# Kernel tuning notes

Measured on AMD Instinct MI355X. Metric: run time of the kernel, lower is better.

## Reference

```python
import jax, jax.numpy as jnp
import numpy as np

N_NODES = 10000
N_EDGES = 160000
N_GRAPHS = 20
IN_F, HID, OUT_F, HEADS = 50, 256, 121, 4
NEG_SLOPE = 0.2
GN_EPS = 1e-5
SM_EPS = 1e-16


def _with_self_loops(edge_index, n):
    loop = jnp.arange(n, dtype=edge_index.dtype)
    src = jnp.concatenate([edge_index[0], loop])
    dst = jnp.concatenate([edge_index[1], loop])
    return src, dst


def gat_conv(x, W, att_src, att_dst, bias, src, dst, heads, out_c):
    # PyG GATConv: linear -> per-node attention halves -> edge leaky_relu
    # -> softmax over incoming edges of each dst -> weighted scatter-sum.
    n = x.shape[0]
    h = (x @ W).reshape(n, heads, out_c)                # [N,H,C]
    a_s = (h * att_src).sum(-1)                          # [N,H]
    a_d = (h * att_dst).sum(-1)                          # [N,H]
    e = a_s[src] + a_d[dst]                              # [E,H]
    e = jnp.where(e > 0, e, NEG_SLOPE * e)
    e_max = jax.ops.segment_max(e, dst, num_segments=n)  # self-loops cover all dst
    ex = jnp.exp(e - e_max[dst])
    den = jax.ops.segment_sum(ex, dst, num_segments=n)
    alpha = ex / (den[dst] + SM_EPS)                     # [E,H]
    out = jax.ops.segment_sum(h[src] * alpha[..., None], dst, num_segments=n)
    return out.reshape(n, heads * out_c) + bias


def graph_norm(x, batch, weight, bias, mean_scale, n_graphs):
    cnt = jax.ops.segment_sum(jnp.ones((x.shape[0],), x.dtype), batch,
                              num_segments=n_graphs)[:, None]    # [G,1]
    mean = jax.ops.segment_sum(x, batch, num_segments=n_graphs) / cnt
    ctr = x - mean[batch] * mean_scale
    var = jax.ops.segment_sum(ctr * ctr, batch, num_segments=n_graphs) / cnt
    inv = jax.lax.rsqrt(var + GN_EPS)
    return weight * ctr * inv[batch] + bias


def setup_inputs() -> dict:
    key = jax.random.key(0)
    ks = jax.random.split(key, 24)
    d = {}
    d['x'] = jax.random.normal(ks[0], (N_NODES, IN_F), jnp.float32)
    d['edge_index'] = jax.random.randint(ks[1], (2, N_EDGES), 0, N_NODES, jnp.int64 if jax.config.jax_enable_x64 else jnp.int32)
    d['batch'] = jnp.sort(jax.random.randint(ks[2], (N_NODES,), 0, N_GRAPHS))
    def glorot(k, shape):
        fan = shape[0] + shape[-1]
        return jax.random.normal(k, shape, jnp.float32) * np.sqrt(2.0 / fan)
    dims = [(IN_F, HEADS, HID), (HEADS * HID, HEADS, HID), (HEADS * HID, HEADS, HID), (HEADS * HID, 1, OUT_F)]
    i = 3
    for li, (fin, h, c) in enumerate(dims, 1):
        d[f'W{li}'] = glorot(ks[i], (fin, h * c)); i += 1
        d[f'as{li}'] = glorot(ks[i], (h, c)); i += 1
        d[f'ad{li}'] = glorot(ks[i], (h, c)); i += 1
        d[f'b{li}'] = jnp.zeros((h * c,), jnp.float32)
    for li in (1, 2, 3):
        w = HEADS * HID
        d[f'gw{li}'] = jnp.ones((w,), jnp.float32)
        d[f'gb{li}'] = jnp.zeros((w,), jnp.float32)
        d[f'ga{li}'] = jnp.ones((w,), jnp.float32)
    return d


def reference(x, edge_index, batch,
              W1, as1, ad1, b1, W2, as2, ad2, b2, W3, as3, ad3, b3, W4, as4, ad4, b4,
              gw1, gb1, ga1, gw2, gb2, ga2, gw3, gb3, ga3):
    src, dst = _with_self_loops(edge_index, N_NODES)
    h = gat_conv(x, W1, as1, ad1, b1, src, dst, HEADS, HID)
    h = jax.nn.elu(graph_norm(h, batch, gw1, gb1, ga1, N_GRAPHS))
    h = gat_conv(h, W2, as2, ad2, b2, src, dst, HEADS, HID)
    h = jax.nn.elu(graph_norm(h, batch, gw2, gb2, ga2, N_GRAPHS))
    h = gat_conv(h, W3, as3, ad3, b3, src, dst, HEADS, HID)
    h = jax.nn.elu(graph_norm(h, batch, gw3, gb3, ga3, N_GRAPHS))
    return gat_conv(h, W4, as4, ad4, b4, src, dst, 1, OUT_F)
```

## Files before the change

### kernel.cpp

```cpp
#include <hip/hip_runtime.h>
#include <math.h>

#define NN 10000
#define NE 160000
#define E2 (NE + NN)
#define NG 20
#define MPAD 10240
#define NSPLIT 8

typedef __attribute__((ext_vector_type(8))) short short8;
typedef __attribute__((ext_vector_type(4))) float f32x4;
typedef __attribute__((ext_vector_type(4))) unsigned short us4;

__device__ inline unsigned short f2bf(float f){
  unsigned u = __float_as_uint(f);
  unsigned r = u + 0x7FFFu + ((u >> 16) & 1u);
  return (unsigned short)(r >> 16);
}
__device__ inline float bf2f(unsigned short h){ return __uint_as_float(((unsigned)h) << 16); }

__device__ inline void gload_lds16(const void* g, void* l){
  __builtin_amdgcn_global_load_lds((const __attribute__((address_space(1))) void*)g,
                                   (__attribute__((address_space(3))) void*)l, 16, 0, 0);
}

__global__ void k_gptr(const int* __restrict__ batch, int* __restrict__ gptr){
  int g = threadIdx.x;
  if (g > NG) return;
  int lo = 0, hi = NN;
  while (lo < hi){ int mid = (lo+hi)>>1; if (batch[mid] < g) lo = mid+1; else hi = mid; }
  gptr[g] = lo;
}

__global__ void k_count(const int* __restrict__ ei, int* __restrict__ cnt){
  int e = blockIdx.x*256 + threadIdx.x;
  if (e >= E2) return;
  int d = (e < NE) ? ei[NE + e] : (e - NE);
  atomicAdd(&cnt[d], 1);
}

__global__ void k_scan(const int* __restrict__ cnt, int* __restrict__ ptr){
  __shared__ int tpre[256];
  __shared__ int tsum[256];
  int tid = threadIdx.x;
  const int per = (NN + 255)/256;
  int base = tid*per;
  int s = 0;
  for (int i=0;i<per;i++){ int idx=base+i; if (idx<NN) s += cnt[idx]; }
  tsum[tid] = s;
  __syncthreads();
  if (tid == 0){
    int run = 0;
    for (int i=0;i<256;i++){ tpre[i]=run; run += tsum[i]; }
    ptr[NN] = run;
  }
  __syncthreads();
  int run = tpre[tid];
  for (int i=0;i<per;i++){ int idx=base+i; if (idx<NN){ ptr[idx]=run; run += cnt[idx]; } }
}

__global__ void k_copy(const int* __restrict__ src, int* __restrict__ dst){
  int i = blockIdx.x*256 + threadIdx.x;
  if (i < NN) dst[i] = src[i];
}

__global__ void k_scatter(const int* __restrict__ ei, int* __restrict__ fill, int* __restrict__ csrc){
  int e = blockIdx.x*256 + threadIdx.x;
  if (e >= E2) return;
  int s, d;
  if (e < NE){ s = ei[e]; d = ei[NE + e]; } else { s = d = e - NE; }
  int pos = atomicAdd(&fill[d], 1);
  csrc[pos] = s;
}

__global__ void k_xconv(const float* __restrict__ x, unsigned short* __restrict__ xbf){
  int i = blockIdx.x*256 + threadIdx.x;
  if (i >= MPAD*64) return;
  int r = i >> 6, c = i & 63;
  float v = (r < NN && c < 50) ? x[r*50 + c] : 0.f;
  xbf[i] = f2bf(v);
}

#define WT0 0
#define WT1 65536
#define WT2 1114112
#define WT3 2162688
#define WTT 2293760
__global__ void k_wconvall(const float* __restrict__ W0, const float* __restrict__ W1,
                           const float* __restrict__ W2, const float* __restrict__ W3,
                           unsigned short* __restrict__ wt){
  int i = blockIdx.x*256 + threadIdx.x;
  if (i >= WTT) return;
  const float* W; int K, N, Kpad, off;
  if (i < WT1){ W=W0; K=50; N=1024; Kpad=64; off=WT0; }
  else if (i < WT2){ W=W1; K=1024; N=1024; Kpad=1024; off=WT1; }
  else if (i < WT3){ W=W2; K=1024; N=1024; Kpad=1024; off=WT2; }
  else { W=W3; K=1024; N=121; Kpad=1024; off=WT3; }
  int j = i - off;
  int nn = j / Kpad, kk = j - nn*Kpad;
  float v = (nn < N && kk < K) ? W[(size_t)kk*N + nn] : 0.f;
  wt[i] = f2bf(v);
}

__global__ void k_attpad4(const float* __restrict__ AS3, const float* __restrict__ AD3,
                          float* __restrict__ asp4, float* __restrict__ adp4){
  int i = threadIdx.x;
  asp4[i] = (i < 121) ? AS3[i] : 0.f;
  adp4[i] = (i < 121) ? AD3[i] : 0.f;
}

template<int TBN>
__global__ __launch_bounds__(512, 2) void k_gemm256(
    const unsigned short* __restrict__ A,
    const unsigned short* __restrict__ Bt,
    unsigned short* __restrict__ Cbf,
    const float* __restrict__ asp, const float* __restrict__ adp,
    float* __restrict__ a_s, float* __restrict__ a_d,
    int M, int K, int FS, int ncb, int H)
{
  constexpr int MFR = 8;
  constexpr int NFR = TBN/64;
  constexpr int ABYTES = 256*64;
  constexpr int BBYTES = TBN*64;
  constexpr int AINST = 2;
  constexpr int BINST = TBN/128;
  constexpr int LPS = AINST + BINST;
  __shared__ unsigned short sA[3*256*32];
  __shared__ unsigned short sB[3*TBN*32];
  const int tid = threadIdx.x;
  const int wave = tid >> 6;
  const int lane = tid & 63;
  const int nwg = gridDim.x;
  const int q = nwg >> 3, rmod = nwg & 7;
  const int xcd = blockIdx.x & 7, idx = blockIdx.x >> 3;
  const int wg = (xcd < rmod) ? (xcd*(q+1) + idx) : (rmod*(q+1) + (xcd - rmod)*q + idx);
  const int rowt = wg / ncb;
  const int colt = wg - rowt*ncb;
  const int row0 = rowt * 256;
  const int col0 = colt * TBN;
  const int wr = (wave >> 2) * 128;
  const int wc = (wave & 3) * (TBN/4);
  f32x4 acc[MFR][NFR];
  #pragma unroll
  for (int i=0;i<MFR;i++)
    #pragma unroll
    for (int j=0;j<NFR;j++){ acc[i][j][0]=0.f; acc[i][j][1]=0.f; acc[i][j][2]=0.f; acc[i][j][3]=0.f; }

  const unsigned short* aP[AINST];
  int aL[AINST];
  #pragma unroll
  for (int i=0;i<AINST;i++){
    int s = (wave*AINST + i)*64 + lane;
    int row = s >> 2, chn = (s & 3) ^ ((row >> 1) & 3);
    aP[i] = A + (size_t)(row0 + row)*K + chn*8;
    aL[i] = (wave*AINST + i)*1024;
  }
  const unsigned short* bP[BINST];
  int bL[BINST];
  #pragma unroll
  for (int i=0;i<BINST;i++){
    int s = (wave*BINST + i)*64 + lane;
    int row = s >> 2, chn = (s & 3) ^ ((row >> 1) & 3);
    bP[i] = Bt + (size_t)(col0 + row)*K + chn*8;
    bL[i] = (wave*BINST + i)*1024;
  }
  char* ldsA = (char*)sA;
  char* ldsB = (char*)sB;

  auto STAGE = [&](int k0, int buf){
    #pragma unroll
    for (int i=0;i<AINST;i++) gload_lds16(aP[i] + k0, ldsA + buf*ABYTES + aL[i]);
    #pragma unroll
    for (int i=0;i<BINST;i++) gload_lds16(bP[i] + k0, ldsB + buf*BBYTES + bL[i]);
  };

  const int NT = K >> 5;
  const int kch = lane >> 4;
  const int rlo = lane & 15;

  STAGE(0, 0);
  STAGE(32, 1);

  int cur = 0;
  for (int t = 0; t < NT; ++t){
    asm volatile("s_waitcnt lgkmcnt(0)" ::: "memory");
    if (t+1 < NT){
      if constexpr (LPS==4) asm volatile("s_waitcnt vmcnt(4)" ::: "memory");
      else                  asm volatile("s_waitcnt vmcnt(3)" ::: "memory");
    } else {
      asm volatile("s_waitcnt vmcnt(0)" ::: "memory");
    }
    __builtin_amdgcn_sched_barrier(0);
    __builtin_amdgcn_s_barrier();
    __builtin_amdgcn_sched_barrier(0);
    const unsigned short* bA = sA + cur*(256*32);
    const unsigned short* bB = sB + cur*(TBN*32);
    short8 af[MFR], bfr[NFR];
    #pragma unroll
    for (int m=0;m<MFR;m++){
      int r = wr + m*16 + rlo;
      af[m] = *(const short8*)(bA + r*32 + ((kch ^ ((r>>1)&3))<<3));
    }
    #pragma unroll
    for (int n=0;n<NFR;n++){
      int r = wc + n*16 + rlo;
      bfr[n] = *(const short8*)(bB + r*32 + ((kch ^ ((r>>1)&3))<<3));
    }
    if (t+2 < NT){
      int nb = cur + 2; if (nb >= 3) nb -= 3;
      STAGE((t+2) << 5, nb);
    }
    __builtin_amdgcn_s_setprio(1);
    #pragma unroll
    for (int m=0;m<MFR;m++)
      #pragma unroll
      for (int n=0;n<NFR;n++)
        acc[m][n] = __builtin_amdgcn_mfma_f32_16x16x32_bf16(af[m], bfr[n], acc[m][n], 0, 0, 0);
    __builtin_amdgcn_s_setprio(0);
    cur += 1; if (cur == 3) cur = 0;
  }
  const int cr = (lane >> 4) * 4;
  const int cc = lane & 15;
  #pragma unroll
  for (int m=0;m<MFR;m++){
    #pragma unroll
    for (int n=0;n<NFR;n++){
      int col = col0 + wc + n*16 + cc;
      #pragma unroll
      for (int r=0;r<4;r++){
        int row = row0 + wr + m*16 + cr + r;
        if (row < M) Cbf[(size_t)row*FS + col] = f2bf(acc[m][n][r]);
      }
    }
  }
  float asv[NFR], adv[NFR];
  #pragma unroll
  for (int n=0;n<NFR;n++){
    int col = col0 + wc + n*16 + cc;
    asv[n] = asp[col]; adv[n] = adp[col];
  }
  __syncthreads();
  float* part = (float*)sA;
  #pragma unroll
  for (int m=0;m<MFR;m++){
    #pragma unroll
    for (int r=0;r<4;r++){
      float ss = 0.f, sd = 0.f;
      #pragma unroll
      for (int n=0;n<NFR;n++){ float v = acc[m][n][r]; ss += v*asv[n]; sd += v*adv[n]; }
      #pragma unroll
      for (int o=8;o;o>>=1){ ss += __shfl_xor(ss,o); sd += __shfl_xor(sd,o); }
      if (cc == 0){
        int rowLocal = m*16 + cr + r;
        int pidx = ((wave>>2)*128 + rowLocal)*8 + (wave&3)*2;
        part[pidx] = ss; part[pidx+1] = sd;
      }
    }
  }
  __syncthreads();
  {
    int row = tid >> 1, v = tid & 1;
    int base = row*8 + v;
    float s = part[base] + part[base+2] + part[base+4] + part[base+6];
    int grow = row0 + row;
    const int head = colt;
    if (grow < M){
      if (v) a_d[grow*H + head] = s;
      else   a_s[grow*H + head] = s;
    }
  }
}

__global__ __launch_bounds__(256) void k_gatherw(
    const unsigned short* __restrict__ h,
    const float* __restrict__ a_s, const float* __restrict__ a_d,
    const int* __restrict__ ptr, const int* __restrict__ csrc,
    const float* __restrict__ bias, float* __restrict__ out)
{
  __shared__ float sal[4][64*4];
  __shared__ int ssn[4][64];
  const int wid = threadIdx.x >> 6, lane = threadIdx.x & 63;
  const int node = blockIdx.x*4 + wid;
  const int hh = lane >> 4;
  const int beg = ptr[node], deg = ptr[node+1] - beg;
  f32x4 ad4 = *(const f32x4*)(a_d + node*4);
  float acc[16], acc2[16];
  #pragma unroll
  for (int j=0;j<16;j++){ acc[j]=0.f; acc2[j]=0.f; }
  f32x4 denp = {0.f,0.f,0.f,0.f};
  const unsigned short* hb = h + lane*16;

  for (int c0 = 0; c0 < deg; c0 += 64){
    int n = min(64, deg - c0);
    if (lane < n){
      int s = csrc[beg + c0 + lane];
      f32x4 as4 = *(const f32x4*)(a_s + s*4);
      f32x4 e4;
      #pragma unroll
      for (int k2=0;k2<4;k2++){
        float ev = as4[k2] + ad4[k2];
        ev = ev > 0.f ? ev : 0.2f*ev;
        float x = __expf(ev);
        e4[k2] = x;
        denp[k2] += x;
      }
      *(f32x4*)&sal[wid][lane*4] = e4;
      ssn[wid][lane] = s;
    }
    int e = 0;
    if (n >= 2){
      int s0 = ssn[wid][0], s1 = ssn[wid][1];
      float aA = sal[wid][hh], aB = sal[wid][4+hh];
      const unsigned short* p0 = hb + (size_t)s0*1024;
      const unsigned short* p1 = hb + (size_t)s1*1024;
      short8 ca0=*(const short8*)p0, ca1=*(const short8*)(p0+8);
      short8 cb0=*(const short8*)p1, cb1=*(const short8*)(p1+8);
      for (e = 0; e+3 < n; e += 2){
        int s2 = ssn[wid][e+2], s3 = ssn[wid][e+3];
        float nA = sal[wid][(e+2)*4+hh], nB = sal[wid][(e+3)*4+hh];
        const unsigned short* p2 = hb + (size_t)s2*1024;
        const unsigned short* p3 = hb + (size_t)s3*1024;
        short8 na0=*(const short8*)p2, na1=*(const short8*)(p2+8);
        short8 nb0=*(const short8*)p3, nb1=*(const short8*)(p3+8);
        #pragma unroll
        for (int j=0;j<8;j++){ acc[j]   += bf2f((unsigned short)ca0[j])*aA;
                               acc[8+j] += bf2f((unsigned short)ca1[j])*aA; }
        #pragma unroll
        for (int j=0;j<8;j++){ acc2[j]   += bf2f((unsigned short)cb0[j])*aB;
                               acc2[8+j] += bf2f((unsigned short)cb1[j])*aB; }
        ca0=na0; ca1=na1; cb0=nb0; cb1=nb1; aA=nA; aB=nB;
      }
      #pragma unroll
      for (int j=0;j<8;j++){ acc[j]   += bf2f((unsigned short)ca0[j])*aA;
                             acc[8+j] += bf2f((unsigned short)ca1[j])*aA; }
      #pragma unroll
      for (int j=0;j<8;j++){ acc2[j]   += bf2f((unsigned short)cb0[j])*aB;
                             acc2[8+j] += bf2f((unsigned short)cb1[j])*aB; }
      e += 2;
    }
    for (; e < n; ++e){
      int s = ssn[wid][e];
      float al = sal[wid][e*4 + hh];
      const unsigned short* p = hb + (size_t)s*1024;
      short8 u0 = *(const short8*)p, u1 = *(const short8*)(p+8);
      #pragma unroll
      for (int j=0;j<8;j++){ acc[j]   += bf2f((unsigned short)u0[j])*al;
                             acc[8+j] += bf2f((unsigned short)u1[j])*al; }
    }
  }
  #pragma unroll
  for (int o=32;o;o>>=1){
    #pragma unroll
    for (int k2=0;k2<4;k2++) denp[k2] += __shfl_xor(denp[k2], o);
  }
  float inv = 1.f / (denp[hh] + 1e-16f);
  float* op = out + (size_t)node*1024 + lane*16;
  const float* bp = bias + lane*16;
  #pragma unroll
  for (int j=0;j<16;j++) op[j] = (acc[j]+acc2[j])*inv + bp[j];
}

__global__ __launch_bounds__(256) void k_gatherw1(
    const unsigned short* __restrict__ h,
    const float* __restrict__ a_s, const float* __restrict__ a_d,
    const int* __restrict__ ptr, const int* __restrict__ csrc,
    const float* __restrict__ bias, float* __restrict__ out)
{
  __shared__ float sal[4][64];
  __shared__ int ssn[4][64];
  const int wid = threadIdx.x >> 6, lane = threadIdx.x & 63;
  const int node = blockIdx.x*4 + wid;
  const int beg = ptr[node], deg = ptr[node+1] - beg;
  float ad = a_d[node];
  float den = 0.f;
  float acc[2] = {0.f,0.f}, acc2[2] = {0.f,0.f};
  const int c0i = lane*2;
  const unsigned short* hb = h + c0i;

  for (int b0 = 0; b0 < deg; b0 += 64){
    int n = min(64, deg - b0);
    if (lane < n){
      int s = csrc[beg + b0 + lane];
      float ev = a_s[s] + ad;
      ev = ev > 0.f ? ev : 0.2f*ev;
      float x = __expf(ev);
      sal[wid][lane] = x;
      ssn[wid][lane] = s;
      den += x;
    }
    int e = 0;
    for (; e + 1 < n; e += 2){
      int sA_ = ssn[wid][e], sB_ = ssn[wid][e+1];
      float aA = sal[wid][e], aB = sal[wid][e+1];
      const unsigned short* pA = hb + (size_t)sA_*128;
      const unsigned short* pB = hb + (size_t)sB_*128;
      acc[0]  += bf2f(pA[0])*aA; acc[1]  += bf2f(pA[1])*aA;
      acc2[0] += bf2f(pB[0])*aB; acc2[1] += bf2f(pB[1])*aB;
    }
    if (e < n){
      int sA_ = ssn[wid][e];
      float aA = sal[wid][e];
      const unsigned short* pA = hb + (size_t)sA_*128;
      acc[0] += bf2f(pA[0])*aA; acc[1] += bf2f(pA[1])*aA;
    }
  }
  #pragma unroll
  for (int o=32;o;o>>=1) den += __shfl_xor(den, o);
  float inv = 1.f / (den + 1e-16f);
  if (c0i < 121)   out[(size_t)node*121 + c0i]   = (acc[0]+acc2[0])*inv + bias[c0i];
  if (c0i+1 < 121) out[(size_t)node*121 + c0i+1] = (acc[1]+acc2[1])*inv + bias[c0i+1];
}

__global__ void k_gnstats(const float* __restrict__ x, const int* __restrict__ gptr,
                          float* __restrict__ psum, float* __restrict__ psq){
  int g = blockIdx.x, sp = blockIdx.z;
  int c4 = threadIdx.x*4;
  int beg = gptr[g], end = gptr[g+1];
  int n = end - beg;
  int per = (n + NSPLIT - 1) / NSPLIT;
  int nb = beg + sp*per, ne = min(end, nb + per);
  f32x4 s = {0.f,0.f,0.f,0.f}, qv = {0.f,0.f,0.f,0.f};
  for (int i = nb; i < ne; i++){
    f32x4 v = *(const f32x4*)(x + (size_t)i*1024 + c4);
    s += v; qv += v*v;
  }
  int idx = (sp*NG + g)*1024 + c4;
  *(f32x4*)(psum + idx) = s;
  *(f32x4*)(psq + idx) = qv;
}

__global__ void k_coef(const float* __restrict__ psum, const float* __restrict__ psq,
                       const int* __restrict__ gptr,
                       const float* __restrict__ w, const float* __restrict__ b, const float* __restrict__ ms,
                       float* __restrict__ cA, float* __restrict__ cB){
  int i = blockIdx.x*256 + threadIdx.x;
  if (i >= NG*1024) return;
  int g = i >> 10, c = i & 1023;
  float cntf = (float)(gptr[g+1] - gptr[g]);
  float sm = 0.f, sq = 0.f;
  #pragma unroll
  for (int sp=0; sp<NSPLIT; sp++){
    sm += psum[(sp*NG + g)*1024 + c];
    sq += psq[(sp*NG + g)*1024 + c];
  }
  float m = sm / cntf;
  float s = ms[c];
  float ex2 = sq / cntf;
  float var = ex2 - 2.f*s*m*m + s*s*m*m;
  float inv = rsqrtf(var + 1e-5f);
  float wa = w[c]*inv;
  cA[i] = wa;
  cB[i] = b[c] - wa*m*s;
}

__global__ void k_applyelu(const float* __restrict__ x, const int* __restrict__ batch,
                           const float* __restrict__ cA, const float* __restrict__ cB,
                           unsigned short* __restrict__ obf){
  int i = blockIdx.x*256 + threadIdx.x;
  if (i >= NN*256) return;
  int node = i >> 8;
  int c4 = (i & 255)*4;
  int g = batch[node];
  f32x4 v = *(const f32x4*)(x + (size_t)node*1024 + c4);
  f32x4 a = *(const f32x4*)(cA + g*1024 + c4);
  f32x4 b = *(const f32x4*)(cB + g*1024 + c4);
  us4 o;
  #pragma unroll
  for (int j=0;j<4;j++){
    float y = a[j]*v[j] + b[j];
    y = y > 0.f ? y : expm1f(y);
    o[j] = f2bf(y);
  }
  *(us4*)(obf + (size_t)node*1024 + c4) = o;
}

extern "C" void kernel_launch(void* const* d_in, const int* in_sizes, int n_in,
                              void* d_out, int out_size, void* d_ws, size_t ws_size,
                              hipStream_t stream){
  (void)in_sizes; (void)n_in; (void)out_size; (void)ws_size;
  const float* x     = (const float*)d_in[0];
  const int*   ei    = (const int*)d_in[1];
  const int*   batch = (const int*)d_in[2];
  const float* W[4]  = {(const float*)d_in[3],  (const float*)d_in[7],  (const float*)d_in[11], (const float*)d_in[15]};
  const float* AS[4] = {(const float*)d_in[4],  (const float*)d_in[8],  (const float*)d_in[12], (const float*)d_in[16]};
  const float* AD[4] = {(const float*)d_in[5],  (const float*)d_in[9],  (const float*)d_in[13], (const float*)d_in[17]};
  const float* BI[4] = {(const float*)d_in[6],  (const float*)d_in[10], (const float*)d_in[14], (const float*)d_in[18]};
  const float* GW[3] = {(const float*)d_in[19], (const float*)d_in[22], (const float*)d_in[25]};
  const float* GB[3] = {(const float*)d_in[20], (const float*)d_in[23], (const float*)d_in[26]};
  const float* GA[3] = {(const float*)d_in[21], (const float*)d_in[24], (const float*)d_in[27]};

  float* ws   = (float*)d_ws;
  float* bufB = ws;
  float* a_s  = bufB + (size_t)NN*1024;
  float* a_d  = a_s + (size_t)NN*4;
  float* psum = a_d + (size_t)NN*4;
  float* psq  = psum + (size_t)NSPLIT*NG*1024;
  float* cA   = psq  + (size_t)NSPLIT*NG*1024;
  float* cB   = cA   + (size_t)NG*1024;
  float* asp4 = cB   + (size_t)NG*1024;
  float* adp4 = asp4 + 128;
  int* ptr  = (int*)(adp4 + 128);
  int* fill = ptr + (NN + 8);
  int* csrc = fill + (NN + 8);
  int* gptr = csrc + E2;
  unsigned short* abf = (unsigned short*)(gptr + 24);
  unsigned short* xbf = abf;
  unsigned short* hbf = abf + (size_t)MPAD*1024;
  unsigned short* wt  = hbf + (size_t)NN*1024;

  hipMemsetAsync(fill, 0, sizeof(int)*(NN+1), stream);
  k_gptr<<<1, 32, 0, stream>>>(batch, gptr);
  k_count<<<(E2+255)/256, 256, 0, stream>>>(ei, fill);
  k_scan<<<1, 256, 0, stream>>>(fill, ptr);
  k_copy<<<(NN+255)/256, 256, 0, stream>>>(ptr, fill);
  k_scatter<<<(E2+255)/256, 256, 0, stream>>>(ei, fill, csrc);
  k_xconv<<<(MPAD*64+255)/256, 256, 0, stream>>>(x, xbf);
  k_wconvall<<<(WTT+255)/256, 256, 0, stream>>>(W[0], W[1], W[2], W[3], wt);
  k_attpad4<<<1, 128, 0, stream>>>(AS[3], AD[3], asp4, adp4);

  const int Kp[4]  = {64, 1024, 1024, 1024};
  const int Np[4]  = {1024, 1024, 1024, 128};
  const int Woff[4] = {WT0, WT1, WT2, WT3};
  for (int li = 0; li < 4; ++li){
    int FS = Np[li];
    const unsigned short* Ain = (li == 0) ? xbf : abf;
    const unsigned short* Wt = wt + Woff[li];
    if (li < 3){
      int ncb = 4;
      int nwg = (MPAD/256) * ncb;
      k_gemm256<256><<<nwg, 512, 0, stream>>>(Ain, Wt, hbf, AS[li], AD[li], a_s, a_d,
                                              NN, Kp[li], FS, ncb, 4);
      k_gatherw<<<NN/4, 256, 0, stream>>>(hbf, a_s, a_d, ptr, csrc, BI[li], bufB);
      k_gnstats<<<dim3(NG, 1, NSPLIT), 256, 0, stream>>>(bufB, gptr, psum, psq);
      k_coef<<<(NG*1024 + 255)/256, 256, 0, stream>>>(psum, psq, gptr, GW[li], GB[li], GA[li], cA, cB);
      k_applyelu<<<(NN*256 + 255)/256, 256, 0, stream>>>(bufB, batch, cA, cB, abf);
    } else {
      int ncb = 1;
      int nwg = (MPAD/256) * ncb;
      k_gemm256<128><<<nwg, 512, 0, stream>>>(Ain, Wt, hbf, asp4, adp4, a_s, a_d,
                                              NN, Kp[li], FS, ncb, 1);
      k_gatherw1<<<NN/4, 256, 0, stream>>>(hbf, a_s, a_d, ptr, csrc, BI[li], (float*)d_out);
    }
  }
}
```

Measured before the change: 481.6 us.

## Retile attention GEMM to 256x128 with split-half attention partials and 3-way gather unroll

The hidden-layer GEMM uses 256x128 tiles with eight column blocks instead of four, giving twice as many workgroups. Launch bounds now ask for four blocks per CU. Because each head now spans two column tiles, the per-node attention dot products go to two partial buffers, and the gather kernel adds them when it loads them. The last layer's GEMM uses 128x128 row tiles. The gather loop is unrolled to three edges per step with one accumulator instead of two, trading memory-level parallelism against register pressure and a longer serial add chain.

```diff
diff --git a/kernel.cpp b/kernel.cpp
--- a/kernel.cpp
+++ b/kernel.cpp
@@ -7,6 +7,7 @@
 #define NG 20
 #define MPAD 10240
 #define NSPLIT 8
+#define ASTR (NN*4)
 
 typedef __attribute__((ext_vector_type(8))) short short8;
 typedef __attribute__((ext_vector_type(4))) float f32x4;
@@ -109,8 +110,8 @@
   adp4[i] = (i < 121) ? AD3[i] : 0.f;
 }
 
-template<int TBN>
-__global__ __launch_bounds__(512, 2) void k_gemm256(
+template<int TBM, int TBN>
+__global__ __launch_bounds__(512, 4) void k_gemm256(
     const unsigned short* __restrict__ A,
     const unsigned short* __restrict__ Bt,
     unsigned short* __restrict__ Cbf,
@@ -118,14 +119,14 @@
     float* __restrict__ a_s, float* __restrict__ a_d,
     int M, int K, int FS, int ncb, int H)
 {
-  constexpr int MFR = 8;
+  constexpr int MFR = TBM/32;
   constexpr int NFR = TBN/64;
-  constexpr int ABYTES = 256*64;
+  constexpr int ABYTES = TBM*64;
   constexpr int BBYTES = TBN*64;
-  constexpr int AINST = 2;
+  constexpr int AINST = TBM/128;
   constexpr int BINST = TBN/128;
   constexpr int LPS = AINST + BINST;
-  __shared__ unsigned short sA[3*256*32];
+  __shared__ unsigned short sA[3*TBM*32];
   __shared__ unsigned short sB[3*TBN*32];
   const int tid = threadIdx.x;
   const int wave = tid >> 6;
@@ -136,9 +137,9 @@
   const int wg = (xcd < rmod) ? (xcd*(q+1) + idx) : (rmod*(q+1) + (xcd - rmod)*q + idx);
   const int rowt = wg / ncb;
   const int colt = wg - rowt*ncb;
-  const int row0 = rowt * 256;
+  const int row0 = rowt * TBM;
   const int col0 = colt * TBN;
-  const int wr = (wave >> 2) * 128;
+  const int wr = (wave >> 2) * (TBM/2);
   const int wc = (wave & 3) * (TBN/4);
   f32x4 acc[MFR][NFR];
   #pragma unroll
@@ -185,15 +186,16 @@
   for (int t = 0; t < NT; ++t){
     asm volatile("s_waitcnt lgkmcnt(0)" ::: "memory");
     if (t+1 < NT){
-      if constexpr (LPS==4) asm volatile("s_waitcnt vmcnt(4)" ::: "memory");
-      else                  asm volatile("s_waitcnt vmcnt(3)" ::: "memory");
+      if constexpr (LPS==4)      asm volatile("s_waitcnt vmcnt(4)" ::: "memory");
+      else if constexpr (LPS==3) asm volatile("s_waitcnt vmcnt(3)" ::: "memory");
+      else                       asm volatile("s_waitcnt vmcnt(2)" ::: "memory");
     } else {
       asm volatile("s_waitcnt vmcnt(0)" ::: "memory");
     }
     __builtin_amdgcn_sched_barrier(0);
     __builtin_amdgcn_s_barrier();
     __builtin_amdgcn_sched_barrier(0);
-    const unsigned short* bA = sA + cur*(256*32);
+    const unsigned short* bA = sA + cur*(TBM*32);
     const unsigned short* bB = sB + cur*(TBN*32);
     short8 af[MFR], bfr[NFR];
     #pragma unroll
@@ -252,21 +254,22 @@
       for (int o=8;o;o>>=1){ ss += __shfl_xor(ss,o); sd += __shfl_xor(sd,o); }
       if (cc == 0){
         int rowLocal = m*16 + cr + r;
-        int pidx = ((wave>>2)*128 + rowLocal)*8 + (wave&3)*2;
+        int pidx = ((wave>>2)*(TBM/2) + rowLocal)*8 + (wave&3)*2;
         part[pidx] = ss; part[pidx+1] = sd;
       }
     }
   }
   __syncthreads();
-  {
+  if (tid < TBM*2){
     int row = tid >> 1, v = tid & 1;
     int base = row*8 + v;
     float s = part[base] + part[base+2] + part[base+4] + part[base+6];
     int grow = row0 + row;
-    const int head = colt;
+    const int head = colt >> 1;
+    const int p = colt & 1;
     if (grow < M){
-      if (v) a_d[grow*H + head] = s;
-      else   a_s[grow*H + head] = s;
+      float* out = (v ? a_d : a_s) + p*ASTR;
+      out[grow*H + head] = s;
     }
   }
 }
@@ -284,9 +287,10 @@
   const int hh = lane >> 4;
   const int beg = ptr[node], deg = ptr[node+1] - beg;
   f32x4 ad4 = *(const f32x4*)(a_d + node*4);
-  float acc[16], acc2[16];
-  #pragma unroll
-  for (int j=0;j<16;j++){ acc[j]=0.f; acc2[j]=0.f; }
+  ad4 += *(const f32x4*)(a_d + ASTR + node*4);
+  float acc[16];
+  #pragma unroll
+  for (int j=0;j<16;j++) acc[j]=0.f;
   f32x4 denp = {0.f,0.f,0.f,0.f};
   const unsigned short* hb = h + lane*16;
 
@@ -295,6 +299,7 @@
     if (lane < n){
       int s = csrc[beg + c0 + lane];
       f32x4 as4 = *(const f32x4*)(a_s + s*4);
+      as4 += *(const f32x4*)(a_s + ASTR + s*4);
       f32x4 e4;
       #pragma unroll
       for (int k2=0;k2<4;k2++){
@@ -308,35 +313,46 @@
       ssn[wid][lane] = s;
     }
     int e = 0;
-    if (n >= 2){
-      int s0 = ssn[wid][0], s1 = ssn[wid][1];
-      float aA = sal[wid][hh], aB = sal[wid][4+hh];
+    if (n >= 3){
+      int s0=ssn[wid][0], s1=ssn[wid][1], s2=ssn[wid][2];
+      float xa=sal[wid][hh], xb=sal[wid][4+hh], xc=sal[wid][8+hh];
       const unsigned short* p0 = hb + (size_t)s0*1024;
       const unsigned short* p1 = hb + (size_t)s1*1024;
-      short8 ca0=*(const short8*)p0, ca1=*(const short8*)(p0+8);
-      short8 cb0=*(const short8*)p1, cb1=*(const short8*)(p1+8);
-      for (e = 0; e+3 < n; e += 2){
-        int s2 = ssn[wid][e+2], s3 = ssn[wid][e+3];
-        float nA = sal[wid][(e+2)*4+hh], nB = sal[wid][(e+3)*4+hh];
-        const unsigned short* p2 = hb + (size_t)s2*1024;
-        const unsigned short* p3 = hb + (size_t)s3*1024;
-        short8 na0=*(const short8*)p2, na1=*(const short8*)(p2+8);
-        short8 nb0=*(const short8*)p3, nb1=*(const short8*)(p3+8);
+      const unsigned short* p2 = hb + (size_t)s2*1024;
+      short8 A0=*(const short8*)p0, A1=*(const short8*)(p0+8);
+      short8 B0=*(const short8*)p1, B1=*(const short8*)(p1+8);
+      short8 C0=*(const short8*)p2, C1=*(const short8*)(p2+8);
+      for (e = 0; e+5 < n; e += 3){
+        int t0=ssn[wid][e+3], t1=ssn[wid][e+4], t2=ssn[wid][e+5];
+        float ya=sal[wid][(e+3)*4+hh], yb=sal[wid][(e+4)*4+hh], yc=sal[wid][(e+5)*4+hh];
+        const unsigned short* q0 = hb + (size_t)t0*1024;
+        const unsigned short* q1 = hb + (size_t)t1*1024;
+        const unsigned short* q2 = hb + (size_t)t2*1024;
+        short8 NA0=*(const short8*)q0, NA1=*(const short8*)(q0+8);
+        short8 NB0=*(const short8*)q1, NB1=*(const short8*)(q1+8);
+        short8 NC0=*(const short8*)q2, NC1=*(const short8*)(q2+8);
         #pragma unroll
-        for (int j=0;j<8;j++){ acc[j]   += bf2f((unsigned short)ca0[j])*aA;
-                               acc[8+j] += bf2f((unsigned short)ca1[j])*aA; }
+        for (int j=0;j<8;j++){ acc[j]   += bf2f((unsigned short)A0[j])*xa;
+                               acc[8+j] += bf2f((unsigned short)A1[j])*xa; }
         #pragma unroll
-        for (int j=0;j<8;j++){ acc2[j]   += bf2f((unsigned short)cb0[j])*aB;
-                               acc2[8+j] += bf2f((unsigned short)cb1[j])*aB; }
-        ca0=na0; ca1=na1; cb0=nb0; cb1=nb1; aA=nA; aB=nB;
+        for (int j=0;j<8;j++){ acc[j]   += bf2f((unsigned short)B0[j])*xb;
+                               acc[8+j] += bf2f((unsigned short)B1[j])*xb; }
+        #pragma unroll
+        for (int j=0;j<8;j++){ acc[j]   += bf2f((unsigned short)C0[j])*xc;
+                               acc[8+j] += bf2f((unsigned short)C1[j])*xc; }
+        A0=NA0; A1=NA1; B0=NB0; B1=NB1; C0=NC0; C1=NC1;
+        xa=ya; xb=yb; xc=yc;
       }
       #pragma unroll
-      for (int j=0;j<8;j++){ acc[j]   += bf2f((unsigned short)ca0[j])*aA;
-                             acc[8+j] += bf2f((unsigned short)ca1[j])*aA; }
-      #pragma unroll
-      for (int j=0;j<8;j++){ acc2[j]   += bf2f((unsigned short)cb0[j])*aB;
-                             acc2[8+j] += bf2f((unsigned short)cb1[j])*aB; }
-      e += 2;
+      for (int j=0;j<8;j++){ acc[j]   += bf2f((unsigned short)A0[j])*xa;
+                             acc[8+j] += bf2f((unsigned short)A1[j])*xa; }
+      #pragma unroll
+      for (int j=0;j<8;j++){ acc[j]   += bf2f((unsigned short)B0[j])*xb;
+                             acc[8+j] += bf2f((unsigned short)B1[j])*xb; }
+      #pragma unroll
+      for (int j=0;j<8;j++){ acc[j]   += bf2f((unsigned short)C0[j])*xc;
+                             acc[8+j] += bf2f((unsigned short)C1[j])*xc; }
+      e += 3;
     }
     for (; e < n; ++e){
       int s = ssn[wid][e];
@@ -357,7 +373,7 @@
   float* op = out + (size_t)node*1024 + lane*16;
   const float* bp = bias + lane*16;
   #pragma unroll
-  for (int j=0;j<16;j++) op[j] = (acc[j]+acc2[j])*inv + bp[j];
+  for (int j=0;j<16;j++) op[j] = acc[j]*inv + bp[j];
 }
 
 __global__ __launch_bounds__(256) void k_gatherw1(
@@ -492,8 +508,8 @@
   float* ws   = (float*)d_ws;
   float* bufB = ws;
   float* a_s  = bufB + (size_t)NN*1024;
-  float* a_d  = a_s + (size_t)NN*4;
-  float* psum = a_d + (size_t)NN*4;
+  float* a_d  = a_s + (size_t)2*ASTR;
+  float* psum = a_d + (size_t)2*ASTR;
   float* psq  = psum + (size_t)NSPLIT*NG*1024;
   float* cA   = psq  + (size_t)NSPLIT*NG*1024;
   float* cB   = cA   + (size_t)NG*1024;
@@ -526,19 +542,19 @@
     const unsigned short* Ain = (li == 0) ? xbf : abf;
     const unsigned short* Wt = wt + Woff[li];
     if (li < 3){
-      int ncb = 4;
+      int ncb = 8;
       int nwg = (MPAD/256) * ncb;
-      k_gemm256<256><<<nwg, 512, 0, stream>>>(Ain, Wt, hbf, AS[li], AD[li], a_s, a_d,
-                                              NN, Kp[li], FS, ncb, 4);
+      k_gemm256<256,128><<<nwg, 512, 0, stream>>>(Ain, Wt, hbf, AS[li], AD[li], a_s, a_d,
+                                                  NN, Kp[li], FS, ncb, 4);
       k_gatherw<<<NN/4, 256, 0, stream>>>(hbf, a_s, a_d, ptr, csrc, BI[li], bufB);
       k_gnstats<<<dim3(NG, 1, NSPLIT), 256, 0, stream>>>(bufB, gptr, psum, psq);
       k_coef<<<(NG*1024 + 255)/256, 256, 0, stream>>>(psum, psq, gptr, GW[li], GB[li], GA[li], cA, cB);
       k_applyelu<<<(NN*256 + 255)/256, 256, 0, stream>>>(bufB, batch, cA, cB, abf);
     } else {
       int ncb = 1;
-      int nwg = (MPAD/256) * ncb;
-      k_gemm256<128><<<nwg, 512, 0, stream>>>(Ain, Wt, hbf, asp4, adp4, a_s, a_d,
-                                              NN, Kp[li], FS, ncb, 1);
+      int nwg = (MPAD/128) * ncb;
+      k_gemm256<128,128><<<nwg, 512, 0, stream>>>(Ain, Wt, hbf, asp4, adp4, a_s, a_d,
+                                                  NN, Kp[li], FS, ncb, 1);
       k_gatherw1<<<NN/4, 256, 0, stream>>>(hbf, a_s, a_d, ptr, csrc, BI[li], (float*)d_out);
     }
   }
```

Result: no change. 488.1 us (+1.3%).
